# Kernel optimization log

Measured on AMD Instinct MI355X. Metric: run time of the kernel, lower is better.

Reference implementation:

```python
import jax, jax.numpy as jnp
import numpy as np

B, S, D, H = 2, 2048, 1024, 16
HD = D // H


def setup_inputs() -> dict:
    key = jax.random.key(0)
    ks = jax.random.split(key, 9)
    x = jax.random.normal(ks[0], (B, S, D), dtype=jnp.float32)
    scale = 1.0 / np.sqrt(D)
    Wq = jax.random.normal(ks[1], (D, D), dtype=jnp.float32) * scale
    bq = jnp.zeros((D,), dtype=jnp.float32)
    Wk = jax.random.normal(ks[2], (D, D), dtype=jnp.float32) * scale
    bk = jnp.zeros((D,), dtype=jnp.float32)
    Wv = jax.random.normal(ks[3], (D, D), dtype=jnp.float32) * scale
    bv = jnp.zeros((D,), dtype=jnp.float32)
    Wo = jax.random.normal(ks[4], (D, D), dtype=jnp.float32) * scale
    bo = jnp.zeros((D,), dtype=jnp.float32)
    return {"x": x, "Wq": Wq, "bq": bq, "Wk": Wk, "bk": bk,
            "Wv": Wv, "bv": bv, "Wo": Wo, "bo": bo}


def reference(x, Wq, bq, Wk, bk, Wv, bv, Wo, bo):
    b, s, d = x.shape
    h, hd = H, HD
    # torch Linear: y = x @ W.T + b
    q = (x @ Wq.T + bq).reshape(b, s, h, hd).transpose(0, 2, 1, 3)  # (b,h,s,hd)
    k = (x @ Wk.T + bk).reshape(b, s, h, hd).transpose(0, 2, 1, 3)
    v = (x @ Wv.T + bv).reshape(b, s, h, hd).transpose(0, 2, 1, 3)
    scores = jnp.einsum('bhqd,bhkd->bhqk', q, k) / np.sqrt(hd)  # (b,h,s,s)
    # FAITHFUL to source: softmax over dim=1 (head axis), not the key axis.
    attn = jax.nn.softmax(scores, axis=1)
    # dropout is identity at inference
    out = jnp.einsum('bhqk,bhkd->bhqd', attn, v)  # (b,h,s,hd)
    out = out.transpose(0, 2, 1, 3).reshape(b, s, d)
    return out @ Wo.T + bo
```

## Files before the change

kernel.cpp:

```cpp
#include <hip/hip_runtime.h>
#include <hip/hip_bf16.h>
#include <cstdint>
#include <cstddef>


typedef __bf16 bf16x8 __attribute__((ext_vector_type(8)));
typedef __bf16 bf16x4 __attribute__((ext_vector_type(4)));
typedef _Float16 f16x2 __attribute__((ext_vector_type(2)));
typedef _Float16 f16x4 __attribute__((ext_vector_type(4)));
typedef _Float16 f16x8 __attribute__((ext_vector_type(8)));
typedef float floatx4 __attribute__((ext_vector_type(4)));

#define S_LEN 2048
#define DIM 1024
#define NH 16
#define HD 64
#define MTOT 4096
#define C_EXP 0.1803368801111244f

__device__ __forceinline__ float fast_exp2(float x) { return __builtin_amdgcn_exp2f(x); }

__device__ __forceinline__ f16x2 pk_cvt(float a, float b) {
    return __builtin_bit_cast(f16x2, __builtin_amdgcn_cvt_pkrtz(a, b));
}

__device__ __forceinline__ void g2l16(const void* g, void* l) {
    __builtin_amdgcn_global_load_lds(
        (const __attribute__((address_space(1))) void*)g,
        (__attribute__((address_space(3))) void*)l, 16, 0, 0);
}

__global__ void cast_all(const float* __restrict__ x,
                         const float* __restrict__ w0, const float* __restrict__ w1,
                         const float* __restrict__ w2, const float* __restrict__ w3,
                         __bf16* __restrict__ xb,
                         __bf16* __restrict__ o0, __bf16* __restrict__ o1,
                         __bf16* __restrict__ o2, _Float16* __restrict__ o3) {
    int bid = blockIdx.x;
    if (bid < 4096) {
        int i = (bid * 256 + threadIdx.x) * 4;
        float4 v = *(const float4*)&x[i];
        bf16x4 o;
        o.x = (__bf16)v.x; o.y = (__bf16)v.y; o.z = (__bf16)v.z; o.w = (__bf16)v.w;
        *(bf16x4*)&xb[i] = o;
        return;
    }
    bid -= 4096;
    int wi = bid >> 10;
    int i = ((bid & 1023) * 256 + threadIdx.x) * 4;
    if (wi == 3) {
        float4 v = *(const float4*)&w3[i];
        f16x4 o;
        o[0] = (_Float16)v.x; o[1] = (_Float16)v.y; o[2] = (_Float16)v.z; o[3] = (_Float16)v.w;
        *(f16x4*)&o3[i] = o;
        return;
    }
    const float* s = (wi == 0) ? w0 : (wi == 1) ? w1 : w2;
    __bf16* d = (wi == 0) ? o0 : (wi == 1) ? o1 : o2;
    float4 v = *(const float4*)&s[i];
    bf16x4 o;
    o.x = (__bf16)v.x; o.y = (__bf16)v.y; o.z = (__bf16)v.z; o.w = (__bf16)v.w;
    *(bf16x4*)&d[i] = o;
}

__global__ __launch_bounds__(256, 2) void qkv_gemm(const __bf16* __restrict__ A,
                                                   const __bf16* __restrict__ Wq,
                                                   const __bf16* __restrict__ Wk,
                                                   const __bf16* __restrict__ Wv,
                                                   const float* __restrict__ bq,
                                                   const float* __restrict__ bk,
                                                   const float* __restrict__ bv,
                                                   __bf16* __restrict__ Qo,
                                                   __bf16* __restrict__ Ko,
                                                   _Float16* __restrict__ Vt) {
    const int tng = blockIdx.x * 128, tm = blockIdx.y * 128;
    const int wsel = tng >> 10, tn = tng & 1023;
    const __bf16* W = (wsel == 0) ? Wq : (wsel == 1) ? Wk : Wv;
    const float* bias = (wsel == 0) ? bq : (wsel == 1) ? bk : bv;
    __shared__ __bf16 As[128 * 32];
    __shared__ __bf16 Bs[128 * 32];
    const int tid = threadIdx.x, wid = tid >> 6, lane = tid & 63;
    const int l15 = lane & 15, quad = lane >> 4;
    const int wm = (wid >> 1) * 64, wn = (wid & 1) * 64;
    floatx4 acc[4][4] = {};
    for (int k0 = 0; k0 < DIM; k0 += 32) {
        __syncthreads();
#pragma unroll
        for (int i = 0; i < 2; ++i) {
            int slot = i * 256 + tid;
            int r = slot >> 2, c8 = (slot & 3) * 8;
            g2l16(&A[(size_t)(tm + r) * DIM + k0 + c8], &As[slot * 8]);
            g2l16(&W[(size_t)(tn + r) * DIM + k0 + c8], &Bs[slot * 8]);
        }
        __syncthreads();
        bf16x8 af[4], bf[4];
#pragma unroll
        for (int t = 0; t < 4; ++t) {
            af[t] = *(const bf16x8*)&As[(wm + t * 16 + l15) * 32 + quad * 8];
            bf[t] = *(const bf16x8*)&Bs[(wn + t * 16 + l15) * 32 + quad * 8];
        }
#pragma unroll
        for (int im = 0; im < 4; ++im)
#pragma unroll
            for (int in = 0; in < 4; ++in)
                acc[im][in] = __builtin_amdgcn_mfma_f32_16x16x32_bf16(af[im], bf[in], acc[im][in], 0, 0, 0);
    }
    if (wsel < 2) {
        __bf16* O = wsel ? Ko : Qo;
#pragma unroll
        for (int im = 0; im < 4; ++im)
#pragma unroll
            for (int in = 0; in < 4; ++in)
#pragma unroll
                for (int r = 0; r < 4; ++r) {
                    int row = tm + wm + im * 16 + quad * 4 + r;
                    int col = tn + wn + in * 16 + l15;
                    O[(size_t)row * DIM + col] = (__bf16)(acc[im][in][r] + bias[col]);
                }
    } else {
#pragma unroll
        for (int im = 0; im < 4; ++im)
#pragma unroll
            for (int in = 0; in < 4; ++in) {
                int cv = tn + wn + in * 16 + l15;
                int row4 = tm + wm + im * 16 + quad * 4;
                float bv_ = bias[cv];
                f16x4 o;
#pragma unroll
                for (int r = 0; r < 4; ++r) o[r] = (_Float16)(acc[im][in][r] + bv_);
                *(f16x4*)&Vt[(size_t)cv * MTOT + row4] = o;
            }
    }
}

__global__ __launch_bounds__(512, 8) void den8(const __bf16* __restrict__ Q,
                                               const __bf16* __restrict__ Km,
                                               _Float16* __restrict__ rd) {
    const int kt = blockIdx.x * 64, qt = blockIdx.y * 128, b = blockIdx.z;
    __shared__ __bf16 Ks[2][2 * 2 * 64 * 32];
    const int tid = threadIdx.x, wid = tid >> 6, lane = tid & 63;
    const int l15 = lane & 15, quad = lane >> 4;
    const int kswz = ((lane >> 1) & 3) << 3;
    const int wq = wid * 16;
    floatx4 dsum[4] = {};
    const size_t qrow = (size_t)(b * S_LEN + qt + wq + l15) * DIM;
    const size_t kbase = (size_t)(b * S_LEN + kt) * DIM;

#pragma unroll
    for (int i = 0; i < 2; ++i) {
        int slot = i * 512 + tid;
        int hs = slot >> 9, rem = slot & 511;
        int p = rem >> 8, rem2 = rem & 255;
        int r = rem2 >> 2;
        int c8 = (((rem2 & 3) ^ ((rem2 >> 3) & 3)) * 8);
        g2l16(&Km[kbase + (size_t)r * DIM + hs * HD + p * 32 + c8], &Ks[0][slot * 8]);
    }
    for (int hh = 0; hh < 8; ++hh) {
        const int cur = hh & 1, nxt = cur ^ 1;
        __syncthreads();
        bf16x8 af[2][2];
#pragma unroll
        for (int hs = 0; hs < 2; ++hs) {
            af[hs][0] = *(const bf16x8*)&Q[qrow + (hh * 2 + hs) * HD + quad * 8];
            af[hs][1] = *(const bf16x8*)&Q[qrow + (hh * 2 + hs) * HD + 32 + quad * 8];
        }
        if (hh + 1 < 8) {
#pragma unroll
            for (int i = 0; i < 2; ++i) {
                int slot = i * 512 + tid;
                int hs = slot >> 9, rem = slot & 511;
                int p = rem >> 8, rem2 = rem & 255;
                int r = rem2 >> 2;
                int c8 = (((rem2 & 3) ^ ((rem2 >> 3) & 3)) * 8);
                g2l16(&Km[kbase + (size_t)r * DIM + ((hh + 1) * 2 + hs) * HD + p * 32 + c8],
                      &Ks[nxt][slot * 8]);
            }
        }
#pragma unroll
        for (int hs = 0; hs < 2; ++hs) {
#pragma unroll
            for (int n = 0; n < 4; ++n) {
                bf16x8 b0 = *(const bf16x8*)&Ks[cur][hs * 4096 + (n * 16 + l15) * 32 + ((quad * 8) ^ kswz)];
                bf16x8 b1 = *(const bf16x8*)&Ks[cur][hs * 4096 + 2048 + (n * 16 + l15) * 32 + ((quad * 8) ^ kswz)];
                floatx4 acc = {};
                acc = __builtin_amdgcn_mfma_f32_16x16x32_bf16(af[hs][0], b0, acc, 0, 0, 0);
                acc = __builtin_amdgcn_mfma_f32_16x16x32_bf16(af[hs][1], b1, acc, 0, 0, 0);
                floatx4 sc = acc * C_EXP;
                floatx4 e;
#pragma unroll
                for (int r = 0; r < 4; ++r) e[r] = fast_exp2(sc[r]);
                dsum[n] += e;
            }
        }
    }
#pragma unroll
    for (int n = 0; n < 4; ++n)
#pragma unroll
        for (int r = 0; r < 4; ++r) {
            int q = qt + wq + quad * 4 + r;
            int k = kt + n * 16 + l15;
            rd[(size_t)(b * S_LEN + q) * S_LEN + k] = (_Float16)(1.0f / dsum[n][r]);
        }
}

__global__ __launch_bounds__(512, 6) void attn8(const __bf16* __restrict__ Q,
                                                const __bf16* __restrict__ Km,
                                                const _Float16* __restrict__ Vt,
                                                const _Float16* __restrict__ rd,
                                                _Float16* __restrict__ AO1,
                                                _Float16* __restrict__ AO2) {
    const int qt = (blockIdx.x >> 1) * 128, ks = blockIdx.x & 1;
    const int h0 = blockIdx.y * 2, b = blockIdx.z;
    __shared__ __bf16 Ks[2][2 * 2 * 64 * 32];
    __shared__ _Float16 Vts[2 * 64 * 72];
    const int tid = threadIdx.x, wid = tid >> 6, lane = tid & 63;
    const int l15 = lane & 15, quad = lane >> 4;
    const int kswz = ((lane >> 1) & 3) << 3;
    const int wq = wid * 16;
    const size_t qrow = (size_t)(b * S_LEN + qt + wq + l15) * DIM + h0 * HD;
    bf16x8 qf[2][2];
    qf[0][0] = *(const bf16x8*)&Q[qrow + quad * 8];
    qf[0][1] = *(const bf16x8*)&Q[qrow + 32 + quad * 8];
    qf[1][0] = *(const bf16x8*)&Q[qrow + HD + quad * 8];
    qf[1][1] = *(const bf16x8*)&Q[qrow + HD + 32 + quad * 8];
    const _Float16* rdrow = &rd[(size_t)(b * S_LEN + qt + wq + l15) * S_LEN];
    floatx4 oacc[2][4] = {};
    const int kt0 = ks * (S_LEN / 2);
    const size_t kdim = (size_t)b * S_LEN * DIM;
    const int vr = tid >> 3, vc = (tid & 7) * 8;

#define STAGE_K(BUF, KT_)                                                            \
    {                                                                                \
        _Pragma("unroll")                                                            \
        for (int i = 0; i < 2; ++i) {                                                \
            int slot = i * 512 + tid;                                                \
            int hh = slot >> 9, rem = slot & 511;                                    \
            int p = rem >> 8, rem2 = rem & 255;                                      \
            int r = rem2 >> 2;                                                       \
            int c8 = (((rem2 & 3) ^ ((rem2 >> 3) & 3)) * 8);                         \
            g2l16(&Km[kdim + (size_t)((KT_) + r) * DIM + (h0 + hh) * HD + p * 32 + c8], \
                  &Ks[BUF][slot * 8]);                                               \
        }                                                                            \
    }

    {
        f16x8 v0 = *(const f16x8*)&Vt[(size_t)(h0 * HD + vr) * MTOT + b * S_LEN + kt0 + vc];
        f16x8 v1 = *(const f16x8*)&Vt[(size_t)((h0 + 1) * HD + vr) * MTOT + b * S_LEN + kt0 + vc];
        STAGE_K(0, kt0);
        *(f16x8*)&Vts[vr * 72 + vc] = v0;
        *(f16x8*)&Vts[4608 + vr * 72 + vc] = v1;
    }
    for (int it = 0; it < 16; ++it) {
        const int cur = it & 1, nxt = cur ^ 1;
        const int kt = kt0 + it * 64;
        __syncthreads();
        f16x4 rv[4];
#pragma unroll
        for (int mp = 0; mp < 4; ++mp)
            rv[mp] = *(const f16x4*)&rdrow[kt + mp * 16 + quad * 4];
        f16x8 vt0, vt1;
        const bool has_next = (it + 1 < 16);
        if (has_next) {
            const int ktn = kt + 64;
            vt0 = *(const f16x8*)&Vt[(size_t)(h0 * HD + vr) * MTOT + b * S_LEN + ktn + vc];
            vt1 = *(const f16x8*)&Vt[(size_t)((h0 + 1) * HD + vr) * MTOT + b * S_LEN + ktn + vc];
            STAGE_K(nxt, ktn);
        }
        __builtin_amdgcn_s_setprio(1);
#pragma unroll
        for (int mp = 0; mp < 4; ++mp) {
            const int krow = (mp * 16 + l15) * 32 + ((quad * 8) ^ kswz);
            f16x4 pa[2];
#pragma unroll
            for (int hh = 0; hh < 2; ++hh) {
                bf16x8 kf0 = *(const bf16x8*)&Ks[cur][hh * 4096 + krow];
                bf16x8 kf1 = *(const bf16x8*)&Ks[cur][hh * 4096 + 2048 + krow];
                floatx4 s = {};
                s = __builtin_amdgcn_mfma_f32_16x16x32_bf16(kf0, qf[hh][0], s, 0, 0, 0);
                s = __builtin_amdgcn_mfma_f32_16x16x32_bf16(kf1, qf[hh][1], s, 0, 0, 0);
                floatx4 sc = s * C_EXP;
                f16x2 p01 = pk_cvt(fast_exp2(sc[0]), fast_exp2(sc[1]));
                f16x2 p23 = pk_cvt(fast_exp2(sc[2]), fast_exp2(sc[3]));
                f16x4 p = __builtin_shufflevector(p01, p23, 0, 1, 2, 3);
                pa[hh] = p * rv[mp];
            }
#pragma unroll
            for (int hh = 0; hh < 2; ++hh)
#pragma unroll
                for (int n = 0; n < 4; ++n) {
                    f16x4 vb = *(const f16x4*)&Vts[hh * 4608 + (n * 16 + l15) * 72 + mp * 16 + quad * 4];
                    oacc[hh][n] = __builtin_amdgcn_mfma_f32_16x16x16f16(pa[hh], vb, oacc[hh][n], 0, 0, 0);
                }
        }
        __builtin_amdgcn_s_setprio(0);
        if (has_next) {
            __syncthreads();
            *(f16x8*)&Vts[vr * 72 + vc] = vt0;
            *(f16x8*)&Vts[4608 + vr * 72 + vc] = vt1;
        }
    }
#undef STAGE_K
    _Float16* AO = ks ? AO2 : AO1;
#pragma unroll
    for (int hh = 0; hh < 2; ++hh)
#pragma unroll
        for (int n = 0; n < 4; ++n)
#pragma unroll
            for (int r = 0; r < 4; ++r) {
                int row = qt + wq + quad * 4 + r;
                int col = (h0 + hh) * HD + n * 16 + l15;
                AO[(size_t)(b * S_LEN + row) * DIM + col] = (_Float16)oacc[hh][n][r];
            }
}

__global__ __launch_bounds__(256, 2) void gemm_out2(const _Float16* __restrict__ A1,
                                                    const _Float16* __restrict__ A2,
                                                    const _Float16* __restrict__ Bw,
                                                    const float* __restrict__ bias,
                                                    float* __restrict__ C) {
    const int tm = blockIdx.y * 128, tn = blockIdx.x * 64;
    __shared__ _Float16 As1[2 * 128 * 32];
    __shared__ _Float16 As2[2 * 128 * 32];
    __shared__ _Float16 Bs[2 * 64 * 32];
    const int tid = threadIdx.x, wid = tid >> 6, lane = tid & 63;
    const int l15 = lane & 15, quad = lane >> 4;
    const int wm = (wid >> 1) * 64, wn = (wid & 1) * 32;
    floatx4 acc[4][2] = {};
    for (int k0 = 0; k0 < DIM; k0 += 64) {
        __syncthreads();
#pragma unroll
        for (int i = 0; i < 4; ++i) {
            int slot = i * 256 + tid;
            int p = slot >> 9, rem = slot & 511;
            int r = rem >> 2, c8 = (rem & 3) * 8;
            size_t ga = (size_t)(tm + r) * DIM + k0 + p * 32 + c8;
            g2l16(&A1[ga], &As1[slot * 8]);
            g2l16(&A2[ga], &As2[slot * 8]);
        }
#pragma unroll
        for (int i = 0; i < 2; ++i) {
            int slot = i * 256 + tid;
            int p = slot >> 8, rem = slot & 255;
            int r = rem >> 2, c8 = (rem & 3) * 8;
            g2l16(&Bw[(size_t)(tn + r) * DIM + k0 + p * 32 + c8], &Bs[slot * 8]);
        }
        __syncthreads();
#pragma unroll
        for (int kc = 0; kc < 2; ++kc) {
            f16x8 af[4], bf[2];
#pragma unroll
            for (int t = 0; t < 4; ++t) {
                int off = kc * 4096 + (wm + t * 16 + l15) * 32 + quad * 8;
                f16x8 a1 = *(const f16x8*)&As1[off];
                f16x8 a2 = *(const f16x8*)&As2[off];
                af[t] = a1 + a2;
            }
#pragma unroll
            for (int t = 0; t < 2; ++t)
                bf[t] = *(const f16x8*)&Bs[kc * 2048 + (wn + t * 16 + l15) * 32 + quad * 8];
#pragma unroll
            for (int im = 0; im < 4; ++im)
#pragma unroll
                for (int in = 0; in < 2; ++in)
                    acc[im][in] = __builtin_amdgcn_mfma_f32_16x16x32_f16(af[im], bf[in], acc[im][in], 0, 0, 0);
        }
    }
#pragma unroll
    for (int im = 0; im < 4; ++im)
#pragma unroll
        for (int in = 0; in < 2; ++in)
#pragma unroll
            for (int r = 0; r < 4; ++r) {
                int row = tm + wm + im * 16 + quad * 4 + r;
                int col = tn + wn + in * 16 + l15;
                C[(size_t)row * DIM + col] = acc[im][in][r] + bias[col];
            }
}

extern "C" void kernel_launch(void* const* d_in, const int* in_sizes, int n_in,
                              void* d_out, int out_size, void* d_ws, size_t ws_size,
                              hipStream_t stream) {
    const float* x  = (const float*)d_in[0];
    const float* Wq = (const float*)d_in[1];
    const float* bq = (const float*)d_in[2];
    const float* Wk = (const float*)d_in[3];
    const float* bk = (const float*)d_in[4];
    const float* Wv = (const float*)d_in[5];
    const float* bv = (const float*)d_in[6];
    const float* Wo = (const float*)d_in[7];
    const float* bo = (const float*)d_in[8];
    float* out = (float*)d_out;

    char* ws = (char*)d_ws;
    const size_t MB = 1u << 20;
    __bf16*    xb  = (__bf16*)(ws);
    __bf16*    Wqb = (__bf16*)(ws + 8 * MB);
    __bf16*    Wkb = (__bf16*)(ws + 10 * MB);
    __bf16*    Wvb = (__bf16*)(ws + 12 * MB);
    _Float16*  Wof = (_Float16*)(ws + 14 * MB);
    __bf16*    Qb  = (__bf16*)(ws + 16 * MB);
    __bf16*    Kb  = (__bf16*)(ws + 24 * MB);
    _Float16*  VtH = (_Float16*)(ws + 32 * MB);
    _Float16*  rd  = (_Float16*)(ws + 40 * MB);
    _Float16*  AO1 = (_Float16*)(ws + 56 * MB);
    _Float16*  AO2 = (_Float16*)(ws + 64 * MB);

    cast_all<<<8192, 256, 0, stream>>>(x, Wq, Wk, Wv, Wo, xb, Wqb, Wkb, Wvb, Wof);

    qkv_gemm<<<dim3(24, 32), 256, 0, stream>>>(xb, Wqb, Wkb, Wvb, bq, bk, bv, Qb, Kb, VtH);

    den8<<<dim3(S_LEN / 64, S_LEN / 128, 2), 512, 0, stream>>>(Qb, Kb, rd);

    attn8<<<dim3((S_LEN / 128) * 2, NH / 2, 2), 512, 0, stream>>>(Qb, Kb, VtH, rd, AO1, AO2);

    gemm_out2<<<dim3(DIM / 64, MTOT / 128), 256, 0, stream>>>(AO1, AO2, Wof, bo, out);
}
```

Before: 316.2 us.

## Split attention key range four ways and sum four partials in output GEMM

The attention kernel now splits the key dimension into four chunks instead of two, doubling the grid to raise occupancy and parallelism. Each chunk writes its own fp16 partial output, and a new output GEMM loads all four partials and sums them before the MFMA. A fallback path with double-buffered V tiles and no setprio is kept for small workspaces. The cost is more partial-output traffic and extra LDS in the output GEMM. AO3 reuses the xb region, which is no longer needed by that point.

Result: faster. 280.4 us (-11.3%).

```diff
diff --git a/kernel.cpp b/kernel.cpp
--- a/kernel.cpp
+++ b/kernel.cpp
@@ -203,13 +203,15 @@
         }
 }
 
-__global__ __launch_bounds__(512, 6) void attn8(const __bf16* __restrict__ Q,
-                                                const __bf16* __restrict__ Km,
-                                                const _Float16* __restrict__ Vt,
-                                                const _Float16* __restrict__ rd,
-                                                _Float16* __restrict__ AO1,
-                                                _Float16* __restrict__ AO2) {
-    const int qt = (blockIdx.x >> 1) * 128, ks = blockIdx.x & 1;
+__global__ __launch_bounds__(512, 4) void attn4h(const __bf16* __restrict__ Q,
+                                                 const __bf16* __restrict__ Km,
+                                                 const _Float16* __restrict__ Vt,
+                                                 const _Float16* __restrict__ rd,
+                                                 _Float16* __restrict__ AO1,
+                                                 _Float16* __restrict__ AO2,
+                                                 _Float16* __restrict__ AO3,
+                                                 _Float16* __restrict__ AO4) {
+    const int qt = (blockIdx.x >> 2) * 128, ks = blockIdx.x & 3;
     const int h0 = blockIdx.y * 2, b = blockIdx.z;
     __shared__ __bf16 Ks[2][2 * 2 * 64 * 32];
     __shared__ _Float16 Vts[2 * 64 * 72];
@@ -225,11 +227,11 @@
     qf[1][1] = *(const bf16x8*)&Q[qrow + HD + 32 + quad * 8];
     const _Float16* rdrow = &rd[(size_t)(b * S_LEN + qt + wq + l15) * S_LEN];
     floatx4 oacc[2][4] = {};
-    const int kt0 = ks * (S_LEN / 2);
+    const int kt0 = ks * (S_LEN / 4);
     const size_t kdim = (size_t)b * S_LEN * DIM;
     const int vr = tid >> 3, vc = (tid & 7) * 8;
 
-#define STAGE_K(BUF, KT_)                                                            \
+#define STAGE_K4(BUF, KT_)                                                           \
     {                                                                                \
         _Pragma("unroll")                                                            \
         for (int i = 0; i < 2; ++i) {                                                \
@@ -246,11 +248,11 @@
     {
         f16x8 v0 = *(const f16x8*)&Vt[(size_t)(h0 * HD + vr) * MTOT + b * S_LEN + kt0 + vc];
         f16x8 v1 = *(const f16x8*)&Vt[(size_t)((h0 + 1) * HD + vr) * MTOT + b * S_LEN + kt0 + vc];
-        STAGE_K(0, kt0);
+        STAGE_K4(0, kt0);
         *(f16x8*)&Vts[vr * 72 + vc] = v0;
         *(f16x8*)&Vts[4608 + vr * 72 + vc] = v1;
     }
-    for (int it = 0; it < 16; ++it) {
+    for (int it = 0; it < 8; ++it) {
         const int cur = it & 1, nxt = cur ^ 1;
         const int kt = kt0 + it * 64;
         __syncthreads();
@@ -259,12 +261,12 @@
         for (int mp = 0; mp < 4; ++mp)
             rv[mp] = *(const f16x4*)&rdrow[kt + mp * 16 + quad * 4];
         f16x8 vt0, vt1;
-        const bool has_next = (it + 1 < 16);
+        const bool has_next = (it + 1 < 8);
         if (has_next) {
             const int ktn = kt + 64;
             vt0 = *(const f16x8*)&Vt[(size_t)(h0 * HD + vr) * MTOT + b * S_LEN + ktn + vc];
             vt1 = *(const f16x8*)&Vt[(size_t)((h0 + 1) * HD + vr) * MTOT + b * S_LEN + ktn + vc];
-            STAGE_K(nxt, ktn);
+            STAGE_K4(nxt, ktn);
         }
         __builtin_amdgcn_s_setprio(1);
 #pragma unroll
@@ -299,8 +301,8 @@
             *(f16x8*)&Vts[4608 + vr * 72 + vc] = vt1;
         }
     }
-#undef STAGE_K
-    _Float16* AO = ks ? AO2 : AO1;
+#undef STAGE_K4
+    _Float16* AO = (ks == 0) ? AO1 : (ks == 1) ? AO2 : (ks == 2) ? AO3 : AO4;
 #pragma unroll
     for (int hh = 0; hh < 2; ++hh)
 #pragma unroll
@@ -313,11 +315,190 @@
             }
 }
 
-__global__ __launch_bounds__(256, 2) void gemm_out2(const _Float16* __restrict__ A1,
-                                                    const _Float16* __restrict__ A2,
-                                                    const _Float16* __restrict__ Bw,
-                                                    const float* __restrict__ bias,
-                                                    float* __restrict__ C) {
+__global__ __launch_bounds__(512, 4) void attn2h(const __bf16* __restrict__ Q,
+                                                 const __bf16* __restrict__ Km,
+                                                 const _Float16* __restrict__ Vt,
+                                                 const _Float16* __restrict__ rd,
+                                                 _Float16* __restrict__ AO1,
+                                                 _Float16* __restrict__ AO2) {
+    const int qt = (blockIdx.x >> 1) * 128, ks = blockIdx.x & 1;
+    const int h0 = blockIdx.y * 2, b = blockIdx.z;
+    __shared__ __bf16 Ks[2][2 * 2 * 64 * 32];
+    __shared__ _Float16 Vts[2][2 * 64 * 72];
+    const int tid = threadIdx.x, wid = tid >> 6, lane = tid & 63;
+    const int l15 = lane & 15, quad = lane >> 4;
+    const int kswz = ((lane >> 1) & 3) << 3;
+    const int wq = wid * 16;
+    const size_t qrow = (size_t)(b * S_LEN + qt + wq + l15) * DIM + h0 * HD;
+    bf16x8 qf[2][2];
+    qf[0][0] = *(const bf16x8*)&Q[qrow + quad * 8];
+    qf[0][1] = *(const bf16x8*)&Q[qrow + 32 + quad * 8];
+    qf[1][0] = *(const bf16x8*)&Q[qrow + HD + quad * 8];
+    qf[1][1] = *(const bf16x8*)&Q[qrow + HD + 32 + quad * 8];
+    const _Float16* rdrow = &rd[(size_t)(b * S_LEN + qt + wq + l15) * S_LEN];
+    floatx4 oacc[2][4] = {};
+    const int kt0 = ks * (S_LEN / 2);
+    const size_t kdim = (size_t)b * S_LEN * DIM;
+    const int vr = tid >> 3, vc = (tid & 7) * 8;
+
+#define STAGE_K2(BUF, KT_)                                                           \
+    {                                                                                \
+        _Pragma("unroll")                                                            \
+        for (int i = 0; i < 2; ++i) {                                                \
+            int slot = i * 512 + tid;                                                \
+            int hh = slot >> 9, rem = slot & 511;                                    \
+            int p = rem >> 8, rem2 = rem & 255;                                      \
+            int r = rem2 >> 2;                                                       \
+            int c8 = (((rem2 & 3) ^ ((rem2 >> 3) & 3)) * 8);                         \
+            g2l16(&Km[kdim + (size_t)((KT_) + r) * DIM + (h0 + hh) * HD + p * 32 + c8], \
+                  &Ks[BUF][slot * 8]);                                               \
+        }                                                                            \
+    }
+
+    {
+        f16x8 v0 = *(const f16x8*)&Vt[(size_t)(h0 * HD + vr) * MTOT + b * S_LEN + kt0 + vc];
+        f16x8 v1 = *(const f16x8*)&Vt[(size_t)((h0 + 1) * HD + vr) * MTOT + b * S_LEN + kt0 + vc];
+        STAGE_K2(0, kt0);
+        *(f16x8*)&Vts[0][vr * 72 + vc] = v0;
+        *(f16x8*)&Vts[0][4608 + vr * 72 + vc] = v1;
+    }
+    for (int it = 0; it < 16; ++it) {
+        const int cur = it & 1, nxt = cur ^ 1;
+        const int kt = kt0 + it * 64;
+        __syncthreads();
+        f16x4 rv[4];
+#pragma unroll
+        for (int mp = 0; mp < 4; ++mp)
+            rv[mp] = *(const f16x4*)&rdrow[kt + mp * 16 + quad * 4];
+        f16x8 vt0, vt1;
+        const bool has_next = (it + 1 < 16);
+        if (has_next) {
+            const int ktn = kt + 64;
+            vt0 = *(const f16x8*)&Vt[(size_t)(h0 * HD + vr) * MTOT + b * S_LEN + ktn + vc];
+            vt1 = *(const f16x8*)&Vt[(size_t)((h0 + 1) * HD + vr) * MTOT + b * S_LEN + ktn + vc];
+            STAGE_K2(nxt, ktn);
+        }
+#pragma unroll
+        for (int mp = 0; mp < 4; ++mp) {
+            const int krow = (mp * 16 + l15) * 32 + ((quad * 8) ^ kswz);
+            f16x4 pa[2];
+#pragma unroll
+            for (int hh = 0; hh < 2; ++hh) {
+                bf16x8 kf0 = *(const bf16x8*)&Ks[cur][hh * 4096 + krow];
+                bf16x8 kf1 = *(const bf16x8*)&Ks[cur][hh * 4096 + 2048 + krow];
+                floatx4 s = {};
+                s = __builtin_amdgcn_mfma_f32_16x16x32_bf16(kf0, qf[hh][0], s, 0, 0, 0);
+                s = __builtin_amdgcn_mfma_f32_16x16x32_bf16(kf1, qf[hh][1], s, 0, 0, 0);
+                floatx4 sc = s * C_EXP;
+                f16x2 p01 = pk_cvt(fast_exp2(sc[0]), fast_exp2(sc[1]));
+                f16x2 p23 = pk_cvt(fast_exp2(sc[2]), fast_exp2(sc[3]));
+                f16x4 p = __builtin_shufflevector(p01, p23, 0, 1, 2, 3);
+                pa[hh] = p * rv[mp];
+            }
+#pragma unroll
+            for (int hh = 0; hh < 2; ++hh)
+#pragma unroll
+                for (int n = 0; n < 4; ++n) {
+                    f16x4 vb = *(const f16x4*)&Vts[cur][hh * 4608 + (n * 16 + l15) * 72 + mp * 16 + quad * 4];
+                    oacc[hh][n] = __builtin_amdgcn_mfma_f32_16x16x16f16(pa[hh], vb, oacc[hh][n], 0, 0, 0);
+                }
+        }
+        if (has_next) {
+            *(f16x8*)&Vts[nxt][vr * 72 + vc] = vt0;
+            *(f16x8*)&Vts[nxt][4608 + vr * 72 + vc] = vt1;
+        }
+    }
+#undef STAGE_K2
+    _Float16* AO = ks ? AO2 : AO1;
+#pragma unroll
+    for (int hh = 0; hh < 2; ++hh)
+#pragma unroll
+        for (int n = 0; n < 4; ++n)
+#pragma unroll
+            for (int r = 0; r < 4; ++r) {
+                int row = qt + wq + quad * 4 + r;
+                int col = (h0 + hh) * HD + n * 16 + l15;
+                AO[(size_t)(b * S_LEN + row) * DIM + col] = (_Float16)oacc[hh][n][r];
+            }
+}
+
+__global__ __launch_bounds__(256, 2) void gout4(const _Float16* __restrict__ A1,
+                                                const _Float16* __restrict__ A2,
+                                                const _Float16* __restrict__ A3,
+                                                const _Float16* __restrict__ A4,
+                                                const _Float16* __restrict__ Bw,
+                                                const float* __restrict__ bias,
+                                                float* __restrict__ C) {
+    const int tm = blockIdx.y * 128, tn = blockIdx.x * 64;
+    __shared__ _Float16 As1[2 * 128 * 32];
+    __shared__ _Float16 As2[2 * 128 * 32];
+    __shared__ _Float16 As3[2 * 128 * 32];
+    __shared__ _Float16 As4[2 * 128 * 32];
+    __shared__ _Float16 Bs[2 * 64 * 32];
+    const int tid = threadIdx.x, wid = tid >> 6, lane = tid & 63;
+    const int l15 = lane & 15, quad = lane >> 4;
+    const int wm = (wid >> 1) * 64, wn = (wid & 1) * 32;
+    floatx4 acc[4][2] = {};
+    for (int k0 = 0; k0 < DIM; k0 += 64) {
+        __syncthreads();
+#pragma unroll
+        for (int i = 0; i < 4; ++i) {
+            int slot = i * 256 + tid;
+            int p = slot >> 9, rem = slot & 511;
+            int r = rem >> 2, c8 = (rem & 3) * 8;
+            size_t ga = (size_t)(tm + r) * DIM + k0 + p * 32 + c8;
+            g2l16(&A1[ga], &As1[slot * 8]);
+            g2l16(&A2[ga], &As2[slot * 8]);
+            g2l16(&A3[ga], &As3[slot * 8]);
+            g2l16(&A4[ga], &As4[slot * 8]);
+        }
+#pragma unroll
+        for (int i = 0; i < 2; ++i) {
+            int slot = i * 256 + tid;
+            int p = slot >> 8, rem = slot & 255;
+            int r = rem >> 2, c8 = (rem & 3) * 8;
+            g2l16(&Bw[(size_t)(tn + r) * DIM + k0 + p * 32 + c8], &Bs[slot * 8]);
+        }
+        __syncthreads();
+#pragma unroll
+        for (int kc = 0; kc < 2; ++kc) {
+            f16x8 af[4], bf[2];
+#pragma unroll
+            for (int t = 0; t < 4; ++t) {
+                int off = kc * 4096 + (wm + t * 16 + l15) * 32 + quad * 8;
+                f16x8 a1 = *(const f16x8*)&As1[off];
+                f16x8 a2 = *(const f16x8*)&As2[off];
+                f16x8 a3 = *(const f16x8*)&As3[off];
+                f16x8 a4 = *(const f16x8*)&As4[off];
+                af[t] = (a1 + a2) + (a3 + a4);
+            }
+#pragma unroll
+            for (int t = 0; t < 2; ++t)
+                bf[t] = *(const f16x8*)&Bs[kc * 2048 + (wn + t * 16 + l15) * 32 + quad * 8];
+#pragma unroll
+            for (int im = 0; im < 4; ++im)
+#pragma unroll
+                for (int in = 0; in < 2; ++in)
+                    acc[im][in] = __builtin_amdgcn_mfma_f32_16x16x32_f16(af[im], bf[in], acc[im][in], 0, 0, 0);
+        }
+    }
+#pragma unroll
+    for (int im = 0; im < 4; ++im)
+#pragma unroll
+        for (int in = 0; in < 2; ++in)
+#pragma unroll
+            for (int r = 0; r < 4; ++r) {
+                int row = tm + wm + im * 16 + quad * 4 + r;
+                int col = tn + wn + in * 16 + l15;
+                C[(size_t)row * DIM + col] = acc[im][in][r] + bias[col];
+            }
+}
+
+__global__ __launch_bounds__(256, 2) void gout2(const _Float16* __restrict__ A1,
+                                                const _Float16* __restrict__ A2,
+                                                const _Float16* __restrict__ Bw,
+                                                const float* __restrict__ bias,
+                                                float* __restrict__ C) {
     const int tm = blockIdx.y * 128, tn = blockIdx.x * 64;
     __shared__ _Float16 As1[2 * 128 * 32];
     __shared__ _Float16 As2[2 * 128 * 32];
@@ -404,6 +585,10 @@
     _Float16*  rd  = (_Float16*)(ws + 40 * MB);
     _Float16*  AO1 = (_Float16*)(ws + 56 * MB);
     _Float16*  AO2 = (_Float16*)(ws + 64 * MB);
+    _Float16*  AO3 = (_Float16*)(ws);
+    _Float16*  AO4 = (_Float16*)(ws + 72 * MB);
+
+    const bool four = ws_size >= (size_t)80 * MB;
 
     cast_all<<<8192, 256, 0, stream>>>(x, Wq, Wk, Wv, Wo, xb, Wqb, Wkb, Wvb, Wof);
 
@@ -411,7 +596,12 @@
 
     den8<<<dim3(S_LEN / 64, S_LEN / 128, 2), 512, 0, stream>>>(Qb, Kb, rd);
 
-    attn8<<<dim3((S_LEN / 128) * 2, NH / 2, 2), 512, 0, stream>>>(Qb, Kb, VtH, rd, AO1, AO2);
-
-    gemm_out2<<<dim3(DIM / 64, MTOT / 128), 256, 0, stream>>>(AO1, AO2, Wof, bo, out);
-}
+    if (four) {
+        attn4h<<<dim3((S_LEN / 128) * 4, NH / 2, 2), 512, 0, stream>>>(Qb, Kb, VtH, rd,
+                                                                       AO1, AO2, AO3, AO4);
+        gout4<<<dim3(DIM / 64, MTOT / 128), 256, 0, stream>>>(AO1, AO2, AO3, AO4, Wof, bo, out);
+    } else {
+        attn2h<<<dim3((S_LEN / 128) * 2, NH / 2, 2), 512, 0, stream>>>(Qb, Kb, VtH, rd, AO1, AO2);
+        gout2<<<dim3(DIM / 64, MTOT / 128), 256, 0, stream>>>(AO1, AO2, Wof, bo, out);
+    }
+}
```
